# Kernel tuning notes

Measured on AMD Instinct MI355X. Metric: run time of the kernel, lower is better.

The kernel has to match this reference:

```python
import jax, jax.numpy as jnp
import numpy as np

NEG_INF = float(np.finfo(np.float32).min)
EPS = 1e-6
NOISE_STD = 1.0
CHUNK = 8
TEMP = 1.0


def moving_sum(x, back, forward):
    # x: [B, T]; windowed sum over [t-back, t+forward] via prefix sums (O(T))
    B, T = x.shape
    cs = jnp.concatenate([jnp.zeros((B, 1), x.dtype), jnp.cumsum(x, axis=1)], axis=1)  # [B, T+1]
    idx = jnp.arange(T)
    hi = jnp.clip(idx + forward + 1, 0, T)
    lo = jnp.clip(idx - back, 0, T)
    return cs[:, hi] - cs[:, lo]


def setup_inputs() -> dict:
    key = jax.random.key(0)
    ks = jax.random.split(key, 12)
    B, T, KD, QD, AD, VD = 16, 4000, 512, 512, 512, 512
    s = lambda d: 1.0 / np.sqrt(d)
    return {
        "key": jax.random.normal(ks[0], (B, T, KD), jnp.float32),
        "value": jax.random.normal(ks[1], (B, T, VD), jnp.float32),
        "query": jax.random.normal(ks[2], (B, 1, QD), jnp.float32),
        "mask": jnp.ones((B, 1, T), jnp.int32),
        "w_key_mono": jax.random.normal(ks[3], (KD, AD), jnp.float32) * s(KD),
        "b_key_mono": jnp.zeros((AD,), jnp.float32),
        "w_query_mono": jax.random.normal(ks[4], (QD, AD), jnp.float32) * s(QD),
        "v_mono": jax.random.normal(ks[5], (AD,), jnp.float32) * s(AD),
        "g_mono": jnp.asarray(np.sqrt(1.0 / AD), jnp.float32),  # weight_norm gain init
        "r_mono": jnp.asarray(-4.0, jnp.float32),
        "w_key_chunk": jax.random.normal(ks[6], (KD, AD), jnp.float32) * s(KD),
        "b_key_chunk": jnp.zeros((AD,), jnp.float32),
        "w_query_chunk": jax.random.normal(ks[7], (QD, AD), jnp.float32) * s(QD),
        "v_chunk": jax.random.normal(ks[8], (AD,), jnp.float32) * s(AD),
    }


def _energy(key, query, mask, wk, bk, wq, v, r=None, g=None):
    kproj = jax.nn.relu(key) @ wk + bk          # [B, T, A]
    qproj = query @ wq                           # [B, 1, A]
    if g is not None:  # weight-normalized v
        v = g * v / jnp.linalg.norm(v)
    e = jnp.tanh(kproj + qproj) @ v              # [B, T]
    if r is not None:
        e = e + r
    return jnp.where(mask[:, 0, :] == 0, NEG_INF, e)


def reference(key, value, query, mask, w_key_mono, b_key_mono, w_query_mono, v_mono,
              g_mono, r_mono, w_key_chunk, b_key_chunk, w_query_chunk, v_chunk):
    B, T, _ = key.shape
    e_mono = _energy(key, query, mask, w_key_mono, b_key_mono, w_query_mono,
                     v_mono, r=r_mono, g=g_mono)
    noise = jax.random.normal(jax.random.key(123), e_mono.shape, e_mono.dtype) * NOISE_STD
    p_choose = jax.nn.sigmoid(e_mono + noise)                      # [B, T]
    # safe_cumprod of (1 - p): exp(exclusive cumsum of clipped logs)
    log1mp = jnp.log(jnp.clip(1.0 - p_choose, EPS, 1.0))
    cumprod_1mp = jnp.exp(jnp.cumsum(log1mp, axis=1) - log1mp)     # exclusive
    aw_prev = jnp.zeros((B, T), key.dtype).at[:, 0].set(1.0)       # one-hot at t=0
    alpha = p_choose * cumprod_1mp * jnp.cumsum(
        aw_prev / jnp.clip(cumprod_1mp, EPS, 1.0), axis=1)
    # chunkwise attention
    e_chunk = _energy(key, query, mask, w_key_chunk, b_key_chunk, w_query_chunk, v_chunk)
    e_chunk = e_chunk - jnp.max(e_chunk, axis=1, keepdims=True)
    softmax_exp = jnp.maximum(jnp.exp(e_chunk), 1e-5)
    denom = moving_sum(softmax_exp, CHUNK - 1, 0)
    beta = softmax_exp * moving_sum(alpha * TEMP / denom, 0, CHUNK - 1)
    cv = jnp.einsum('bt,btd->bd', beta, value)[:, None, :]         # [B, 1, V]
    return cv, alpha[..., None]
```

## Files before the change

kernel.cpp:

```cpp
#include <hip/hip_runtime.h>
#include <stdint.h>

typedef unsigned short u16;
typedef unsigned int   u32;

#define T_LEN 4000
#define NEG_INF (-3.4028234663852886e38f)

typedef __bf16 bf16x8 __attribute__((ext_vector_type(8)));
typedef float  f32x4  __attribute__((ext_vector_type(4)));

__device__ __forceinline__ u16 f2bf(float f){
    union { float f; u32 i; } v; v.f = f;
    u32 u = v.i;
    u32 r = (u + 0x7FFFu + ((u >> 16) & 1u)) >> 16;
    return (u16)r;
}
__device__ __forceinline__ float tanh_fast(float x){
    float ax = fabsf(x);
    float a = __expf(-2.0f * ax);
    float t = (1.0f - a) / (1.0f + a);
    return copysignf(t, x);
}
__device__ __forceinline__ u32 rotl32(u32 x, int n){ return (x << n) | (x >> (32 - n)); }

__device__ __forceinline__ void gll16(const void* g, void* l){
    __builtin_amdgcn_global_load_lds(
        (__attribute__((address_space(1))) void*)g,
        (__attribute__((address_space(3))) void*)l, 16, 0, 0);
}

__device__ float jax_noise(u32 idx){
    const u32 k0 = 0u, k1 = 123u;
    const u32 k2 = k0 ^ k1 ^ 0x1BD11BDAu;
    u32 x0 = k0;
    u32 x1 = idx + k1;
#define RND(r) { x0 += x1; x1 = rotl32(x1, r); x1 ^= x0; }
    RND(13) RND(15) RND(26) RND(6)   x0 += k1; x1 += k2 + 1u;
    RND(17) RND(29) RND(16) RND(24)  x0 += k2; x1 += k0 + 2u;
    RND(13) RND(15) RND(26) RND(6)   x0 += k0; x1 += k1 + 3u;
    RND(17) RND(29) RND(16) RND(24)  x0 += k1; x1 += k2 + 4u;
    RND(13) RND(15) RND(26) RND(6)   x0 += k2; x1 += k0 + 5u;
#undef RND
    u32 bits = x0 ^ x1;
    union { u32 i; float f; } u;
    u.i = (bits >> 9) | 0x3F800000u;
    float f01 = u.f - 1.0f;
    const float minval = -0.99999994f;
    float uu = f01 * (1.0f - minval) + minval;
    uu = fmaxf(uu, minval);
    return 1.41421356f * erfinvf(uu);
}

__global__ __launch_bounds__(512) void prep_combined(
    const float* __restrict__ v_mono, const float* __restrict__ g_mono,
    const float* __restrict__ query, const float* __restrict__ wq_mono,
    const float* __restrict__ wq_chunk,
    const float* __restrict__ wk_mono, const float* __restrict__ wk_chunk,
    const float* __restrict__ key,
    float* __restrict__ vn, float* __restrict__ qp_mono, float* __restrict__ qp_chunk,
    u16* __restrict__ Wt, u16* __restrict__ kb,
    float* __restrict__ ezero, float* __restrict__ outcv)
{
    __shared__ float shf[512];
    __shared__ u16 tile[32][33];
    const int blk = blockIdx.x;
    const int tid = threadIdx.x;
    if (blk == 0){
        float v = v_mono[tid];
        shf[tid] = v * v;
        __syncthreads();
        for (int off = 256; off >= 1; off >>= 1){
            if (tid < off) shf[tid] += shf[tid + off];
            __syncthreads();
        }
        float g = g_mono[0];
        vn[tid] = g * v / sqrtf(shf[0]);
    } else if (blk <= 32){
        int b = (blk - 1) >> 1;
        int which = (blk - 1) & 1;
        const float* W = which ? wq_chunk : wq_mono;
        float* out = which ? qp_chunk : qp_mono;
        shf[tid] = query[b * 512 + tid];
        __syncthreads();
        float acc = 0.f;
        for (int k = 0; k < 512; k++) acc += shf[k] * W[k * 512 + tid];
        out[b * 512 + tid] = acc;
    } else if (blk <= 544){
        int idx = blk - 33;
        int kt = (idx & 15) * 32, nt = (idx >> 4) * 32;
        int c = tid & 31, r = tid >> 5;
        const float* src = (nt < 512) ? wk_mono : wk_chunk;
        int nbase = (nt < 512) ? nt : nt - 512;
#pragma unroll
        for (int i = 0; i < 2; i++){
            int kk = r + i * 16;
            tile[kk][c] = f2bf(src[(size_t)(kt + kk) * 512 + nbase + c]);
        }
        __syncthreads();
#pragma unroll
        for (int i = 0; i < 2; i++){
            int nn = r + i * 16;
            Wt[(size_t)(nt + nn) * 512 + kt + c] = tile[c][nn];
        }
    } else if (blk < 608){
        int i = ((blk - 545) * 512 + tid) * 4;
        if (i < 128000){
            float4 z = {0.f, 0.f, 0.f, 0.f};
            *reinterpret_cast<float4*>(ezero + i) = z;
        }
    } else if (blk < 612){
        int i = ((blk - 608) * 512 + tid) * 4;
        float4 z = {0.f, 0.f, 0.f, 0.f};
        *reinterpret_cast<float4*>(outcv + i) = z;
    } else {
        size_t i = ((size_t)(blk - 612) * 512 + tid) * 8;
        float4 a = *reinterpret_cast<const float4*>(key + i);
        float4 b = *reinterpret_cast<const float4*>(key + i + 4);
        uint4 pk;
        pk.x = (u32)f2bf(fmaxf(a.x, 0.f)) | ((u32)f2bf(fmaxf(a.y, 0.f)) << 16);
        pk.y = (u32)f2bf(fmaxf(a.z, 0.f)) | ((u32)f2bf(fmaxf(a.w, 0.f)) << 16);
        pk.z = (u32)f2bf(fmaxf(b.x, 0.f)) | ((u32)f2bf(fmaxf(b.y, 0.f)) << 16);
        pk.w = (u32)f2bf(fmaxf(b.z, 0.f)) | ((u32)f2bf(fmaxf(b.w, 0.f)) << 16);
        *reinterpret_cast<uint4*>(kb + i) = pk;
    }
}

__global__ __launch_bounds__(256) void gemm_energy_pre(
    const u16* __restrict__ kb, const u16* __restrict__ Wt,
    const float* __restrict__ b_mono, const float* __restrict__ b_chunk,
    const float* __restrict__ vnorm, const float* __restrict__ v_chunk,
    const float* __restrict__ qp_mono, const float* __restrict__ qp_chunk,
    float* __restrict__ e_mono, float* __restrict__ e_chunk)
{
    __shared__ __align__(16) u16 As[128 * 32];
    __shared__ __align__(16) u16 Bs[128 * 32];
    const int bid = blockIdx.x;
    const int x = ((bid >> 6) << 3) + (bid & 7);
    if (x >= 500) return;
    const int nT = (bid >> 3) & 7;
    const int g0 = x * 128;
    const bool mono = (nT < 4);
    const int n0 = nT * 128;
    const int tid = threadIdx.x;
    const int lane = tid & 63;
    const int wave = tid >> 6;
    const int wm = wave >> 1, wn = wave & 1;
    const int l15 = lane & 15, quad = lane >> 4;

    f32x4 acc[4][4];
#pragma unroll
    for (int i = 0; i < 4; i++)
#pragma unroll
        for (int j = 0; j < 4; j++)
#pragma unroll
            for (int c = 0; c < 4; c++) acc[i][j][c] = 0.f;

    const u16* aG = kb + (size_t)g0 * 512;
    const u16* bG = Wt + (size_t)n0 * 512;

    for (int k0 = 0; k0 < 512; k0 += 32){
#pragma unroll
        for (int it = 0; it < 2; it++){
            int vid = tid + it * 256;
            int row = vid >> 2;
            int part = vid & 3;
            gll16(aG + (size_t)row * 512 + k0 + part * 8, As + vid * 8);
            gll16(bG + (size_t)row * 512 + k0 + part * 8, Bs + vid * 8);
        }
        __syncthreads();
        bf16x8 af[4], bfr[4];
#pragma unroll
        for (int i = 0; i < 4; i++){
            af[i]  = *reinterpret_cast<const bf16x8*>(&As[(wm * 64 + i * 16 + l15) * 32 + quad * 8]);
            bfr[i] = *reinterpret_cast<const bf16x8*>(&Bs[(wn * 64 + i * 16 + l15) * 32 + quad * 8]);
        }
#pragma unroll
        for (int i = 0; i < 4; i++)
#pragma unroll
            for (int j = 0; j < 4; j++)
                acc[i][j] = __builtin_amdgcn_mfma_f32_16x16x32_bf16(af[i], bfr[j], acc[i][j], 0, 0, 0);
        __syncthreads();
    }

    const float* qp = mono ? qp_mono : qp_chunk;
    float* edst = mono ? e_mono : e_chunk;
    float vv[4], bb[4]; int nc[4];
#pragma unroll
    for (int j = 0; j < 4; j++){
        int ncol = (n0 - (mono ? 0 : 512)) + wn * 64 + j * 16 + l15;
        nc[j] = ncol;
        vv[j] = mono ? vnorm[ncol] : v_chunk[ncol];
        bb[j] = mono ? b_mono[ncol] : b_chunk[ncol];
    }
#pragma unroll
    for (int i = 0; i < 4; i++){
#pragma unroll
        for (int r = 0; r < 4; r++){
            int g = g0 + wm * 64 + i * 16 + quad * 4 + r;
            int bidx = (u32)g / 4000u;
            float s = 0.f;
#pragma unroll
            for (int j = 0; j < 4; j++){
                float x2 = acc[i][j][r] + bb[j] + qp[bidx * 512 + nc[j]];
                s += vv[j] * tanh_fast(x2);
            }
            s += __shfl_xor(s, 1);
            s += __shfl_xor(s, 2);
            s += __shfl_xor(s, 4);
            s += __shfl_xor(s, 8);
            if (l15 == 0) atomicAdd(&edst[g], s);
        }
    }
}

__global__ __launch_bounds__(256) void gemm_energy_f32(
    const float* __restrict__ key, const u16* __restrict__ Wt,
    const float* __restrict__ b_mono, const float* __restrict__ b_chunk,
    const float* __restrict__ vnorm, const float* __restrict__ v_chunk,
    const float* __restrict__ qp_mono, const float* __restrict__ qp_chunk,
    float* __restrict__ e_mono, float* __restrict__ e_chunk)
{
    __shared__ __align__(16) u16 As[128 * 40];
    __shared__ __align__(16) u16 Bs[128 * 40];
    const int tid = threadIdx.x;
    const int g0 = blockIdx.x * 128;
    const int nT = blockIdx.y;
    const bool mono = (nT < 4);
    const int n0 = nT * 128;
    const int lane = tid & 63;
    const int wave = tid >> 6;
    const int wm = wave >> 1, wn = wave & 1;
    const int l15 = lane & 15, quad = lane >> 4;

    f32x4 acc[4][4];
#pragma unroll
    for (int i = 0; i < 4; i++)
#pragma unroll
        for (int j = 0; j < 4; j++)
#pragma unroll
            for (int c = 0; c < 4; c++) acc[i][j][c] = 0.f;

    for (int k0 = 0; k0 < 512; k0 += 32){
        __syncthreads();
#pragma unroll
        for (int it = 0; it < 4; it++){
            int vid = tid + it * 256;
            int row = vid >> 3;
            int c4  = (vid & 7) << 2;
            float4 a = *reinterpret_cast<const float4*>(key + (size_t)(g0 + row) * 512 + k0 + c4);
            u32 p0 = (u32)f2bf(fmaxf(a.x, 0.f)) | ((u32)f2bf(fmaxf(a.y, 0.f)) << 16);
            u32 p1 = (u32)f2bf(fmaxf(a.z, 0.f)) | ((u32)f2bf(fmaxf(a.w, 0.f)) << 16);
            uint2 pk; pk.x = p0; pk.y = p1;
            *reinterpret_cast<uint2*>(&As[row * 40 + c4]) = pk;
        }
#pragma unroll
        for (int it = 0; it < 2; it++){
            int vid = tid + it * 256;
            int row = vid >> 2;
            int cb  = (vid & 3) << 3;
            uint4 b = *reinterpret_cast<const uint4*>(Wt + (size_t)(n0 + row) * 512 + k0 + cb);
            *reinterpret_cast<uint4*>(&Bs[row * 40 + cb]) = b;
        }
        __syncthreads();
        bf16x8 af[4], bfr[4];
#pragma unroll
        for (int i = 0; i < 4; i++){
            af[i]  = *reinterpret_cast<const bf16x8*>(&As[(wm * 64 + i * 16 + l15) * 40 + quad * 8]);
            bfr[i] = *reinterpret_cast<const bf16x8*>(&Bs[(wn * 64 + i * 16 + l15) * 40 + quad * 8]);
        }
#pragma unroll
        for (int i = 0; i < 4; i++)
#pragma unroll
            for (int j = 0; j < 4; j++)
                acc[i][j] = __builtin_amdgcn_mfma_f32_16x16x32_bf16(af[i], bfr[j], acc[i][j], 0, 0, 0);
    }

    const float* qp = mono ? qp_mono : qp_chunk;
    float* edst = mono ? e_mono : e_chunk;
    float vv[4], bb[4]; int nc[4];
#pragma unroll
    for (int j = 0; j < 4; j++){
        int ncol = (n0 - (mono ? 0 : 512)) + wn * 64 + j * 16 + l15;
        nc[j] = ncol;
        vv[j] = mono ? vnorm[ncol] : v_chunk[ncol];
        bb[j] = mono ? b_mono[ncol] : b_chunk[ncol];
    }
#pragma unroll
    for (int i = 0; i < 4; i++){
#pragma unroll
        for (int r = 0; r < 4; r++){
            int g = g0 + wm * 64 + i * 16 + quad * 4 + r;
            int bidx = (u32)g / 4000u;
            float s = 0.f;
#pragma unroll
            for (int j = 0; j < 4; j++){
                float x = acc[i][j][r] + bb[j] + qp[bidx * 512 + nc[j]];
                s += vv[j] * tanh_fast(x);
            }
            s += __shfl_xor(s, 1);
            s += __shfl_xor(s, 2);
            s += __shfl_xor(s, 4);
            s += __shfl_xor(s, 8);
            if (l15 == 0) atomicAdd(&edst[g], s);
        }
    }
}

#define IDX(t) ((t) + ((t) >> 4))

__global__ __launch_bounds__(256) void scan_energy(
    const float* __restrict__ e_mono, const float* __restrict__ e_chunk,
    const int* __restrict__ mask, const float* __restrict__ r_mono,
    float* __restrict__ out_alpha, float* __restrict__ beta)
{
    __shared__ float P[4256];
    __shared__ float AL[4256];
    __shared__ float SE[4256];
    __shared__ float red[256];
    const int b = blockIdx.x;
    const int tid = threadIdx.x;
    const float r = r_mono[0];
    const int t0 = tid * 16;

    float l[16];
    float lsum = 0.f;
#pragma unroll
    for (int i = 0; i < 16; i++){
        int t = t0 + i;
        if (t < T_LEN){
            int fl = b * T_LEN + t;
            float e = e_mono[fl] + r;
            if (mask[fl] == 0) e = NEG_INF;
            float x = e + jax_noise((u32)fl);
            float p = 1.0f / (1.0f + expf(-x));
            P[IDX(t)] = p;
            float om = 1.0f - p;
            om = fminf(fmaxf(om, 1e-6f), 1.0f);
            l[i] = logf(om);
            lsum += l[i];
        } else l[i] = 0.f;
    }
    red[tid] = lsum;
    __syncthreads();
#pragma unroll
    for (int off = 1; off < 256; off <<= 1){
        float v = (tid >= off) ? red[tid - off] : 0.f;
        __syncthreads();
        red[tid] += v;
        __syncthreads();
    }
    float run = red[tid] - lsum;
#pragma unroll
    for (int i = 0; i < 16; i++){
        int t = t0 + i;
        if (t < T_LEN){
            float alpha = P[IDX(t)] * expf(run);
            run += l[i];
            AL[IDX(t)] = alpha;
            out_alpha[b * T_LEN + t] = alpha;
        }
    }

    float ec[16]; float lmax = NEG_INF;
#pragma unroll
    for (int i = 0; i < 16; i++){
        int t = t0 + i;
        if (t < T_LEN){
            int fl = b * T_LEN + t;
            float e = e_chunk[fl];
            if (mask[fl] == 0) e = NEG_INF;
            ec[i] = e;
            lmax = fmaxf(lmax, e);
        } else ec[i] = NEG_INF;
    }
    __syncthreads();
    red[tid] = lmax;
    __syncthreads();
    for (int off = 128; off >= 1; off >>= 1){
        if (tid < off) red[tid] = fmaxf(red[tid], red[tid + off]);
        __syncthreads();
    }
    float m = red[0];
#pragma unroll
    for (int i = 0; i < 16; i++){
        int t = t0 + i;
        if (t < T_LEN) SE[IDX(t)] = fmaxf(expf(ec[i] - m), 1e-5f);
    }
    __syncthreads();
#pragma unroll
    for (int i = 0; i < 16; i++){
        int t = t0 + i;
        if (t < T_LEN){
            float d = 0.f;
            int lo = t - 7; if (lo < 0) lo = 0;
            for (int s = lo; s <= t; s++) d += SE[IDX(s)];
            P[IDX(t)] = AL[IDX(t)] / d;
        }
    }
    __syncthreads();
#pragma unroll
    for (int i = 0; i < 16; i++){
        int t = t0 + i;
        if (t < T_LEN){
            float s2 = 0.f;
            int hi = t + 7; if (hi > T_LEN - 1) hi = T_LEN - 1;
            for (int s = t; s <= hi; s++) s2 += P[IDX(s)];
            beta[b * T_LEN + t] = SE[IDX(t)] * s2;
        }
    }
}

__global__ __launch_bounds__(256) void cv_accum(const float* __restrict__ value,
                                                const float* __restrict__ beta,
                                                float* __restrict__ outcv){
    const int b = blockIdx.x >> 4;
    const int c = blockIdx.x & 15;
    const int tid = threadIdx.x;
    __shared__ float bsh[250];
    int tstart = c * 250;
    if (tid < 250) bsh[tid] = beta[b * T_LEN + tstart + tid];
    __syncthreads();
    int dl = (tid & 127) * 4;
    int trow = tid >> 7;
    float4 a = {0.f, 0.f, 0.f, 0.f};
    for (int t = trow; t < 250; t += 2){
        float bt = bsh[t];
        float4 v = *reinterpret_cast<const float4*>(
            value + (size_t)(b * T_LEN + tstart + t) * 512 + dl);
        a.x += bt * v.x; a.y += bt * v.y; a.z += bt * v.z; a.w += bt * v.w;
    }
    atomicAdd(&outcv[b * 512 + dl + 0], a.x);
    atomicAdd(&outcv[b * 512 + dl + 1], a.y);
    atomicAdd(&outcv[b * 512 + dl + 2], a.z);
    atomicAdd(&outcv[b * 512 + dl + 3], a.w);
}

extern "C" void kernel_launch(void* const* d_in, const int* in_sizes, int n_in,
                              void* d_out, int out_size, void* d_ws, size_t ws_size,
                              hipStream_t stream)
{
    const float* key      = (const float*)d_in[0];
    const float* value    = (const float*)d_in[1];
    const float* query    = (const float*)d_in[2];
    const int*   mask     = (const int*)d_in[3];
    const float* wk_mono  = (const float*)d_in[4];
    const float* bk_mono  = (const float*)d_in[5];
    const float* wq_mono  = (const float*)d_in[6];
    const float* v_mono   = (const float*)d_in[7];
    const float* g_mono   = (const float*)d_in[8];
    const float* r_mono   = (const float*)d_in[9];
    const float* wk_chunk = (const float*)d_in[10];
    const float* bk_chunk = (const float*)d_in[11];
    const float* wq_chunk = (const float*)d_in[12];
    const float* v_chunk  = (const float*)d_in[13];

    float* ws      = (float*)d_ws;
    float* e_mono  = ws;
    float* e_chunk = ws + 64000;
    float* beta    = ws + 136192;
    float* qp_mono = ws + 200192;
    float* qp_chunk= ws + 208384;
    float* vnorm   = ws + 216576;
    u16*   Wt      = (u16*)(ws + 217088);
    u16*   kb      = (u16*)(ws + 479232);

    const size_t NEED = 479232u * 4u + (size_t)64000 * 512 * 2;
    const bool big = ws_size >= NEED;

    prep_combined<<<big ? 8612 : 612, 512, 0, stream>>>(
        v_mono, g_mono, query, wq_mono, wq_chunk, wk_mono, wk_chunk, key,
        vnorm, qp_mono, qp_chunk, Wt, kb, e_mono, (float*)d_out);

    if (big){
        gemm_energy_pre<<<4096, 256, 0, stream>>>(kb, Wt, bk_mono, bk_chunk,
                                                  vnorm, v_chunk, qp_mono, qp_chunk,
                                                  e_mono, e_chunk);
    } else {
        gemm_energy_f32<<<dim3(500, 8), 256, 0, stream>>>(key, Wt, bk_mono, bk_chunk,
                                                          vnorm, v_chunk, qp_mono, qp_chunk,
                                                          e_mono, e_chunk);
    }
    scan_energy<<<16, 256, 0, stream>>>(e_mono, e_chunk, mask, r_mono,
                                        (float*)d_out + 8192, beta);
    cv_accum<<<256, 256, 0, stream>>>(value, beta, (float*)d_out);
}
```

Before: 476.6 us.

## Widen GEMM K-tile with XOR-swizzled LDS, double scan threads, pre-reduce cv atomics

The energy GEMM now loads 64-wide K slices per iteration into LDS with an XOR swizzle, which halves the number of barriers and is meant to avoid LDS bank conflicts on the fragment reads. The scan kernel moves to 512 threads with 8 elements each, shortening each thread's serial work at the cost of a deeper block scan and reduction. cv_accum combines its two row partials in shared memory before the atomics, halving the atomic traffic to global memory. These are independent changes across three kernels, and the larger LDS tiles may lower GEMM occupancy.

Result: no change. 472.7 us (-0.8%).

```diff
diff --git a/kernel.cpp b/kernel.cpp
--- a/kernel.cpp
+++ b/kernel.cpp
@@ -133,8 +133,8 @@
     const float* __restrict__ qp_mono, const float* __restrict__ qp_chunk,
     float* __restrict__ e_mono, float* __restrict__ e_chunk)
 {
-    __shared__ __align__(16) u16 As[128 * 32];
-    __shared__ __align__(16) u16 Bs[128 * 32];
+    __shared__ __align__(16) u16 As[128 * 64];
+    __shared__ __align__(16) u16 Bs[128 * 64];
     const int bid = blockIdx.x;
     const int x = ((bid >> 6) << 3) + (bid & 7);
     if (x >= 500) return;
@@ -159,28 +159,37 @@
     const u16* aG = kb + (size_t)g0 * 512;
     const u16* bG = Wt + (size_t)n0 * 512;
 
-    for (int k0 = 0; k0 < 512; k0 += 32){
-#pragma unroll
-        for (int it = 0; it < 2; it++){
+    for (int k0 = 0; k0 < 512; k0 += 64){
+        __syncthreads();
+#pragma unroll
+        for (int it = 0; it < 4; it++){
             int vid = tid + it * 256;
-            int row = vid >> 2;
-            int part = vid & 3;
-            gll16(aG + (size_t)row * 512 + k0 + part * 8, As + vid * 8);
-            gll16(bG + (size_t)row * 512 + k0 + part * 8, Bs + vid * 8);
-        }
-        __syncthreads();
-        bf16x8 af[4], bfr[4];
-#pragma unroll
-        for (int i = 0; i < 4; i++){
-            af[i]  = *reinterpret_cast<const bf16x8*>(&As[(wm * 64 + i * 16 + l15) * 32 + quad * 8]);
-            bfr[i] = *reinterpret_cast<const bf16x8*>(&Bs[(wn * 64 + i * 16 + l15) * 32 + quad * 8]);
-        }
+            int row = vid >> 3;
+            int sl  = (vid & 7) ^ (row & 7);
+            gll16(aG + (size_t)row * 512 + k0 + sl * 8, As + vid * 8);
+            gll16(bG + (size_t)row * 512 + k0 + sl * 8, Bs + vid * 8);
+        }
+        __syncthreads();
+        bf16x8 af[4][2], bfr[4][2];
 #pragma unroll
         for (int i = 0; i < 4; i++)
 #pragma unroll
+            for (int ks = 0; ks < 2; ks++){
+                int ra = wm * 64 + i * 16 + l15;
+                af[i][ks]  = *reinterpret_cast<const bf16x8*>(
+                    &As[ra * 64 + (((ks * 4 + quad) ^ (ra & 7)) << 3)]);
+                int rb = wn * 64 + i * 16 + l15;
+                bfr[i][ks] = *reinterpret_cast<const bf16x8*>(
+                    &Bs[rb * 64 + (((ks * 4 + quad) ^ (rb & 7)) << 3)]);
+            }
+#pragma unroll
+        for (int i = 0; i < 4; i++)
+#pragma unroll
             for (int j = 0; j < 4; j++)
-                acc[i][j] = __builtin_amdgcn_mfma_f32_16x16x32_bf16(af[i], bfr[j], acc[i][j], 0, 0, 0);
-        __syncthreads();
+#pragma unroll
+                for (int ks = 0; ks < 2; ks++)
+                    acc[i][j] = __builtin_amdgcn_mfma_f32_16x16x32_bf16(
+                        af[i][ks], bfr[j][ks], acc[i][j], 0, 0, 0);
     }
 
     const float* qp = mono ? qp_mono : qp_chunk;
@@ -309,7 +318,7 @@
 
 #define IDX(t) ((t) + ((t) >> 4))
 
-__global__ __launch_bounds__(256) void scan_energy(
+__global__ __launch_bounds__(512) void scan_energy(
     const float* __restrict__ e_mono, const float* __restrict__ e_chunk,
     const int* __restrict__ mask, const float* __restrict__ r_mono,
     float* __restrict__ out_alpha, float* __restrict__ beta)
@@ -317,16 +326,16 @@
     __shared__ float P[4256];
     __shared__ float AL[4256];
     __shared__ float SE[4256];
-    __shared__ float red[256];
+    __shared__ float red[512];
     const int b = blockIdx.x;
     const int tid = threadIdx.x;
     const float r = r_mono[0];
-    const int t0 = tid * 16;
-
-    float l[16];
+    const int t0 = tid * 8;
+
+    float l[8];
     float lsum = 0.f;
 #pragma unroll
-    for (int i = 0; i < 16; i++){
+    for (int i = 0; i < 8; i++){
         int t = t0 + i;
         if (t < T_LEN){
             int fl = b * T_LEN + t;
@@ -344,7 +353,7 @@
     red[tid] = lsum;
     __syncthreads();
 #pragma unroll
-    for (int off = 1; off < 256; off <<= 1){
+    for (int off = 1; off < 512; off <<= 1){
         float v = (tid >= off) ? red[tid - off] : 0.f;
         __syncthreads();
         red[tid] += v;
@@ -352,7 +361,7 @@
     }
     float run = red[tid] - lsum;
 #pragma unroll
-    for (int i = 0; i < 16; i++){
+    for (int i = 0; i < 8; i++){
         int t = t0 + i;
         if (t < T_LEN){
             float alpha = P[IDX(t)] * expf(run);
@@ -362,9 +371,9 @@
         }
     }
 
-    float ec[16]; float lmax = NEG_INF;
-#pragma unroll
-    for (int i = 0; i < 16; i++){
+    float ec[8]; float lmax = NEG_INF;
+#pragma unroll
+    for (int i = 0; i < 8; i++){
         int t = t0 + i;
         if (t < T_LEN){
             int fl = b * T_LEN + t;
@@ -377,19 +386,19 @@
     __syncthreads();
     red[tid] = lmax;
     __syncthreads();
-    for (int off = 128; off >= 1; off >>= 1){
+    for (int off = 256; off >= 1; off >>= 1){
         if (tid < off) red[tid] = fmaxf(red[tid], red[tid + off]);
         __syncthreads();
     }
     float m = red[0];
 #pragma unroll
-    for (int i = 0; i < 16; i++){
+    for (int i = 0; i < 8; i++){
         int t = t0 + i;
         if (t < T_LEN) SE[IDX(t)] = fmaxf(expf(ec[i] - m), 1e-5f);
     }
     __syncthreads();
 #pragma unroll
-    for (int i = 0; i < 16; i++){
+    for (int i = 0; i < 8; i++){
         int t = t0 + i;
         if (t < T_LEN){
             float d = 0.f;
@@ -400,7 +409,7 @@
     }
     __syncthreads();
 #pragma unroll
-    for (int i = 0; i < 16; i++){
+    for (int i = 0; i < 8; i++){
         int t = t0 + i;
         if (t < T_LEN){
             float s2 = 0.f;
@@ -418,6 +427,7 @@
     const int c = blockIdx.x & 15;
     const int tid = threadIdx.x;
     __shared__ float bsh[250];
+    __shared__ float part[512];
     int tstart = c * 250;
     if (tid < 250) bsh[tid] = beta[b * T_LEN + tstart + tid];
     __syncthreads();
@@ -430,10 +440,23 @@
             value + (size_t)(b * T_LEN + tstart + t) * 512 + dl);
         a.x += bt * v.x; a.y += bt * v.y; a.z += bt * v.z; a.w += bt * v.w;
     }
-    atomicAdd(&outcv[b * 512 + dl + 0], a.x);
-    atomicAdd(&outcv[b * 512 + dl + 1], a.y);
-    atomicAdd(&outcv[b * 512 + dl + 2], a.z);
-    atomicAdd(&outcv[b * 512 + dl + 3], a.w);
+    if (trow == 1){
+        part[(tid & 127) * 4 + 0] = a.x;
+        part[(tid & 127) * 4 + 1] = a.y;
+        part[(tid & 127) * 4 + 2] = a.z;
+        part[(tid & 127) * 4 + 3] = a.w;
+    }
+    __syncthreads();
+    if (trow == 0){
+        a.x += part[(tid & 127) * 4 + 0];
+        a.y += part[(tid & 127) * 4 + 1];
+        a.z += part[(tid & 127) * 4 + 2];
+        a.w += part[(tid & 127) * 4 + 3];
+        atomicAdd(&outcv[b * 512 + dl + 0], a.x);
+        atomicAdd(&outcv[b * 512 + dl + 1], a.y);
+        atomicAdd(&outcv[b * 512 + dl + 2], a.z);
+        atomicAdd(&outcv[b * 512 + dl + 3], a.w);
+    }
 }
 
 extern "C" void kernel_launch(void* const* d_in, const int* in_sizes, int n_in,
@@ -481,7 +504,7 @@
                                                           vnorm, v_chunk, qp_mono, qp_chunk,
                                                           e_mono, e_chunk);
     }
-    scan_energy<<<16, 256, 0, stream>>>(e_mono, e_chunk, mask, r_mono,
+    scan_energy<<<16, 512, 0, stream>>>(e_mono, e_chunk, mask, r_mono,
                                         (float*)d_out + 8192, beta);
     cv_accum<<<256, 256, 0, stream>>>(value, beta, (float*)d_out);
 }
```
